# Optimization experiments

Hardware: AMD Instinct MI355X
Metric: run time of the kernel (lower is better)

The kernel has to match this reference:

```python
import jax, jax.numpy as jnp
import numpy as np

N_NODES = 100000
N_EDGES = 1600000
D = 128


def _graph_conv(x, src, dst, norm_src, norm_dst, W, b):
    # DGL GraphConv, norm='both': out = D_dst^{-1/2} A D_src^{-1/2} x W + b
    xs = x * norm_src[:, None]                 # [N, d] scale by src (out-)degree
    agg = jax.ops.segment_sum(xs[src], dst, num_segments=N_NODES)  # SpMM
    hd = agg * norm_dst[:, None]
    return hd @ W + b


def setup_inputs() -> dict:
    key = jax.random.key(0)
    ks = jax.random.split(key, 9)
    h = jax.random.normal(ks[0], (N_NODES, D), dtype=jnp.float32)
    src = jax.random.randint(ks[1], (N_EDGES,), 0, N_NODES, dtype=jnp.int64)
    dst = jax.random.randint(ks[2], (N_EDGES,), 0, N_NODES, dtype=jnp.int64)
    s = 1.0 / np.sqrt(D)
    W0 = jax.random.uniform(ks[3], (D, D), jnp.float32, -s, s)
    b0 = jnp.zeros((D,), jnp.float32)
    W1 = jax.random.uniform(ks[4], (D, D), jnp.float32, -s, s)
    b1 = jnp.zeros((D,), jnp.float32)
    W2 = jax.random.uniform(ks[5], (D, D), jnp.float32, -s, s)
    b2 = jnp.zeros((D,), jnp.float32)
    return {"h": h, "src": src, "dst": dst, "W0": W0, "b0": b0,
            "W1": W1, "b1": b1, "W2": W2, "b2": b2}


def reference(h, src, dst, W0, b0, W1, b1, W2, b2):
    ones = jnp.ones((N_EDGES,), jnp.float32)
    deg_out = jnp.maximum(jax.ops.segment_sum(ones, src, num_segments=N_NODES), 1.0)
    deg_in = jnp.maximum(jax.ops.segment_sum(ones, dst, num_segments=N_NODES), 1.0)
    norm_src = deg_out ** -0.5
    norm_dst = deg_in ** -0.5

    x = jax.nn.relu(_graph_conv(h, src, dst, norm_src, norm_dst, W0, b0))
    x = jax.nn.relu(_graph_conv(x, src, dst, norm_src, norm_dst, W1, b1))
    x = _graph_conv(x, src, dst, norm_src, norm_dst, W2, b2)
    # dgl.mean_nodes over a single graph -> [1, out_size]
    return jnp.mean(x, axis=0, keepdims=True)
```

## Files before the change

kernel.cpp:

```cpp
#include <hip/hip_runtime.h>
#include <hip/hip_fp16.h>

#define N_NODES 100000
#define N_EDGES 1600000
#define D 128
#define SCAN_NB ((N_NODES + 1023) / 1024)
#define CHK 128
#define CHUNK_E (N_EDGES / CHK)
#define HALF_N 50000
#define HALF_U (HALF_N / 4)
#define PP_STRIDE (N_NODES / 4)
#define NSH2 2
#define SH2 (N_NODES / NSH2)
#define SH2_U (SH2 / 4)

typedef _Float16 f16x4 __attribute__((ext_vector_type(4)));
typedef _Float16 f16x8 __attribute__((ext_vector_type(8)));
typedef float f32x4 __attribute__((ext_vector_type(4)));
typedef float f32x2 __attribute__((ext_vector_type(2)));

__global__ __launch_bounds__(256) void
k_hist(const int* __restrict__ src, const int* __restrict__ dst,
       unsigned int* __restrict__ pp) {
    __shared__ unsigned int h[HALF_U];
    int b = blockIdx.x;
    int arr = b >> 8, half = (b >> 7) & 1, c = b & (CHK - 1);
    const int* a = arr ? dst : src;
    int lo = half * HALF_N;
    for (int i = threadIdx.x; i < HALF_U; i += 256) h[i] = 0;
    __syncthreads();
    int e0 = c * CHUNK_E;
    for (int i = e0 + threadIdx.x; i < e0 + CHUNK_E; i += 256) {
        int v = a[i] - lo;
        if ((unsigned)v < HALF_N)
            atomicAdd(&h[v >> 2], 1u << ((v & 3) * 8));
    }
    __syncthreads();
    unsigned int* po = pp + ((size_t)(arr * CHK + c)) * PP_STRIDE + half * HALF_U;
    for (int i = threadIdx.x; i < HALF_U; i += 256) po[i] = h[i];
}

__global__ void k_merge(unsigned int* __restrict__ pp,
                        int* __restrict__ cnt_src, int* __restrict__ cnt_dst) {
    int g = blockIdx.x * blockDim.x + threadIdx.x;
    if (g >= 2 * PP_STRIDE) return;
    int arr = g / PP_STRIDE, u = g % PP_STRIDE;
    unsigned int* p = pp + ((size_t)arr * CHK) * PP_STRIDE + u;
    int s0 = 0, s1 = 0, s2 = 0, s3 = 0;
#pragma unroll 8
    for (int c = 0; c < CHK; c++) {
        unsigned int v = p[(size_t)c * PP_STRIDE];
        p[(size_t)c * PP_STRIDE] =
            (unsigned)s0 | ((unsigned)s1 << 8) | ((unsigned)s2 << 16) | ((unsigned)s3 << 24);
        s0 += v & 255; s1 += (v >> 8) & 255; s2 += (v >> 16) & 255; s3 += (v >> 24) & 255;
    }
    int* cnt = arr ? cnt_dst : cnt_src;
    cnt[4 * u + 0] = s0; cnt[4 * u + 1] = s1; cnt[4 * u + 2] = s2; cnt[4 * u + 3] = s3;
}

__global__ __launch_bounds__(1024) void
k_scan1(const int* __restrict__ cnt_dst, const int* __restrict__ cnt_src,
        int* __restrict__ rpD, int* __restrict__ rpS,
        int* __restrict__ bsD, int* __restrict__ bsS) {
    __shared__ int s[1024];
    int arr = blockIdx.x / SCAN_NB, bb = blockIdx.x % SCAN_NB;
    const int* cnt = arr ? cnt_src : cnt_dst;
    int* rp1 = (arr ? rpS : rpD) + 1;
    int* bs = arr ? bsS : bsD;
    int tid = threadIdx.x;
    int i = bb * 1024 + tid;
    int v = (i < N_NODES) ? cnt[i] : 0;
    s[tid] = v;
    __syncthreads();
    for (int d = 1; d < 1024; d <<= 1) {
        int t = (tid >= d) ? s[tid - d] : 0;
        __syncthreads();
        s[tid] += t;
        __syncthreads();
    }
    if (i < N_NODES) rp1[i] = s[tid];
    if (tid == 1023) bs[bb] = s[1023];
}

__global__ void k_scan2(int* __restrict__ bsD, int* __restrict__ bsS) {
    __shared__ int s[128];
    int* bs = blockIdx.x ? bsS : bsD;
    int tid = threadIdx.x;
    int v = (tid < SCAN_NB) ? bs[tid] : 0;
    s[tid] = v;
    __syncthreads();
    for (int d = 1; d < 128; d <<= 1) {
        int t = (tid >= d) ? s[tid - d] : 0;
        __syncthreads();
        s[tid] += t;
        __syncthreads();
    }
    if (tid < SCAN_NB) bs[tid] = s[tid] - v;
}

__global__ void k_scan3norm(int* __restrict__ rpD, int* __restrict__ rpS,
                            const int* __restrict__ bsD, const int* __restrict__ bsS,
                            const int* __restrict__ cnt_src, const int* __restrict__ cnt_dst,
                            float* __restrict__ ns, float* __restrict__ nd,
                            float* __restrict__ colsum) {
    int i = blockIdx.x * blockDim.x + threadIdx.x;
    if (i >= N_NODES) return;
    rpD[1 + i] += bsD[i >> 10];
    rpS[1 + i] += bsS[i >> 10];
    if (i == 0) { rpD[0] = 0; rpS[0] = 0; }
    if (i < 128) colsum[i] = 0.0f;
    ns[i] = rsqrtf((float)max(cnt_src[i], 1));
    nd[i] = rsqrtf((float)max(cnt_dst[i], 1));
}

__global__ __launch_bounds__(256) void
k_scatter_both(const int* __restrict__ src, const int* __restrict__ dst,
               const int* __restrict__ rpD, const int* __restrict__ rpS,
               const unsigned int* __restrict__ pp, const float* __restrict__ nd,
               int* __restrict__ csr_src, float* __restrict__ csrv) {
    __shared__ unsigned int cur[SH2_U];
    int which = blockIdx.x >> 8;
    int bb = blockIdx.x & 255;
    int sh = bb & 1, c = bb >> 1;
    int lo = sh * SH2;
    for (int i = threadIdx.x; i < SH2_U; i += 256) cur[i] = 0;
    __syncthreads();
    int e0 = c * CHUNK_E;
    if (which == 0) {
        const unsigned int* pre = pp + ((size_t)(CHK + c)) * PP_STRIDE;
        for (int i = e0 + threadIdx.x; i < e0 + CHUNK_E; i += 256) {
            int dfull = dst[i];
            int d = dfull - lo;
            if ((unsigned)d < SH2) {
                int sft = (d & 3) * 8;
                int rank = (atomicAdd(&cur[d >> 2], 1u << sft) >> sft) & 255;
                int p8 = (pre[dfull >> 2] >> ((dfull & 3) * 8)) & 255;
                csr_src[rpD[dfull] + p8 + rank] = src[i];
            }
        }
    } else {
        const unsigned int* pre = pp + (size_t)c * PP_STRIDE;
        for (int i = e0 + threadIdx.x; i < e0 + CHUNK_E; i += 256) {
            int sfull = src[i];
            int s = sfull - lo;
            if ((unsigned)s < SH2) {
                int sft = (s & 3) * 8;
                int rank = (atomicAdd(&cur[s >> 2], 1u << sft) >> sft) & 255;
                int p8 = (pre[sfull >> 2] >> ((sfull & 3) * 8)) & 255;
                csrv[rpS[sfull] + p8 + rank] = nd[dst[i]];
            }
        }
    }
}

__global__ void k_wsum(const int* __restrict__ rpS, const float* __restrict__ csrv,
                       const float* __restrict__ ns, float* __restrict__ wsum) {
    int gid = blockIdx.x * blockDim.x + threadIdx.x;
    int wv = gid >> 6, lane = gid & 63;
    int n = wv * 16 + (lane & 15);
    int off = lane >> 4;
    float s = 0.0f;
    int beg = 0, end = 0;
    if (n < N_NODES) { beg = rpS[n]; end = rpS[n + 1]; }
    for (int j = beg + off; j < end; j += 4) s += csrv[j];
    s += __shfl_xor(s, 16, 64);
    s += __shfl_xor(s, 32, 64);
    if (n < N_NODES && lane < 16) wsum[n] = s * ns[n];
}

__global__ void k_prep(const float* __restrict__ W0, const float* __restrict__ W1,
                       __half* __restrict__ Wt, const float* __restrict__ x,
                       const float* __restrict__ ns, unsigned int* __restrict__ out) {
    if (blockIdx.x < 128) {
        int i = blockIdx.x * 256 + threadIdx.x;
        int l = i >> 14, r = i & (D * D - 1);
        int n = r >> 7, k = r & 127;
        const float* W = l ? W1 : W0;
        Wt[i] = __float2half(W[k * D + n]);
        return;
    }
    int i = (blockIdx.x - 128) * 256 + threadIdx.x;
    if (i >= N_NODES * (D / 4)) return;
    int n = i >> 5;
    float4 v = ((const float4*)x)[i];
    float s = ns[n];
    int u = __builtin_amdgcn_cvt_pk_fp8_f32(v.x * s, v.y * s, 0, false);
    u = __builtin_amdgcn_cvt_pk_fp8_f32(v.z * s, v.w * s, u, true);
    out[i] = (unsigned int)u;
}

__global__ __launch_bounds__(256) void
k_spmm(const unsigned char* __restrict__ x8, const int* __restrict__ row_ptr,
       const int* __restrict__ csr_src, __half* __restrict__ agg) {
    int wave = (blockIdx.x * blockDim.x + threadIdx.x) >> 6;
    int lane = threadIdx.x & 63;
    int hf = lane >> 5, l32 = lane & 31;
    if (wave >= N_NODES) return;
    int beg = row_ptr[wave], end = row_ptr[wave + 1];
    float a0 = 0.f, a1 = 0.f, a2 = 0.f, a3 = 0.f;
    int j = beg;
    for (; j + 7 < end; j += 8) {
#pragma unroll
        for (int p = 0; p < 4; p++) {
            int s0 = csr_src[j + 2 * p];
            int s1 = csr_src[j + 2 * p + 1];
            int s = hf ? s1 : s0;
            unsigned int u = *(const unsigned int*)(x8 + (size_t)s * D + 4 * l32);
            f32x2 lo = __builtin_amdgcn_cvt_pk_f32_fp8(u, false);
            f32x2 hi = __builtin_amdgcn_cvt_pk_f32_fp8(u, true);
            a0 += lo[0]; a1 += lo[1]; a2 += hi[0]; a3 += hi[1];
        }
    }
    for (; j + 1 < end; j += 2) {
        int s0 = csr_src[j], s1 = csr_src[j + 1];
        int s = hf ? s1 : s0;
        unsigned int u = *(const unsigned int*)(x8 + (size_t)s * D + 4 * l32);
        f32x2 lo = __builtin_amdgcn_cvt_pk_f32_fp8(u, false);
        f32x2 hi = __builtin_amdgcn_cvt_pk_f32_fp8(u, true);
        a0 += lo[0]; a1 += lo[1]; a2 += hi[0]; a3 += hi[1];
    }
    if (j < end && hf == 0) {
        int s = csr_src[j];
        unsigned int u = *(const unsigned int*)(x8 + (size_t)s * D + 4 * l32);
        f32x2 lo = __builtin_amdgcn_cvt_pk_f32_fp8(u, false);
        f32x2 hi = __builtin_amdgcn_cvt_pk_f32_fp8(u, true);
        a0 += lo[0]; a1 += lo[1]; a2 += hi[0]; a3 += hi[1];
    }
    a0 += __shfl_xor(a0, 32, 64);
    a1 += __shfl_xor(a1, 32, 64);
    a2 += __shfl_xor(a2, 32, 64);
    a3 += __shfl_xor(a3, 32, 64);
    if (hf == 0) {
        f16x4 o;
        o[0] = (_Float16)a0; o[1] = (_Float16)a1; o[2] = (_Float16)a2; o[3] = (_Float16)a3;
        ((f16x4*)(agg + (size_t)wave * D))[l32] = o;
    }
}

__global__ __launch_bounds__(256) void
k_gemm_mfma(const __half* __restrict__ A, const __half* __restrict__ Wt,
            const float* __restrict__ b, const float* __restrict__ nd,
            const float* __restrict__ ns, unsigned char* __restrict__ out) {
    int w = threadIdx.x >> 6, lane = threadIdx.x & 63;
    int m = lane & 15, q = lane >> 4;
    int row0 = blockIdx.x * 128 + w * 32;

    f16x8 zf;
#pragma unroll
    for (int j = 0; j < 8; j++) zf[j] = (_Float16)0;
    f16x8 af[2][4];
#pragma unroll
    for (int g = 0; g < 2; g++) {
        int arow = row0 + g * 16 + m;
        const f16x8* pa = (const f16x8*)(A + (size_t)arow * D);
        bool aok = arow < N_NODES;
#pragma unroll
        for (int ks = 0; ks < 4; ks++) af[g][ks] = aok ? pa[ks * 4 + q] : zf;
    }

    const f16x8* pb = (const f16x8*)Wt;
    f32x4 acc[2][8];
#pragma unroll
    for (int g = 0; g < 2; g++)
#pragma unroll
        for (int nt = 0; nt < 8; nt++) acc[g][nt] = (f32x4){0.f, 0.f, 0.f, 0.f};

#pragma unroll
    for (int ks = 0; ks < 4; ks++) {
#pragma unroll
        for (int nt = 0; nt < 8; nt++) {
            f16x8 bf = pb[((nt * 16 + m) << 4) + (ks << 2) + q];
            acc[0][nt] = __builtin_amdgcn_mfma_f32_16x16x32_f16(af[0][ks], bf, acc[0][nt], 0, 0, 0);
            acc[1][nt] = __builtin_amdgcn_mfma_f32_16x16x32_f16(af[1][ks], bf, acc[1][nt], 0, 0, 0);
        }
    }

#pragma unroll
    for (int g = 0; g < 2; g++) {
        int er = row0 + g * 16 + q * 4;
        float sd[4], ss[4];
#pragma unroll
        for (int r = 0; r < 4; r++) {
            int n = er + r;
            bool ok = n < N_NODES;
            sd[r] = ok ? nd[n] : 0.0f;
            ss[r] = ok ? ns[n] : 0.0f;
        }
#pragma unroll
        for (int nt = 0; nt < 8; nt++) {
            int col = nt * 16 + m;
            float bc = b[col];
#pragma unroll
            for (int r = 0; r < 4; r++) {
                int n = er + r;
                if (n < N_NODES) {
                    float v = fmaxf(sd[r] * acc[g][nt][r] + bc, 0.0f) * ss[r];
                    int pk = __builtin_amdgcn_cvt_pk_fp8_f32(v, v, 0, false);
                    out[(size_t)n * D + col] = (unsigned char)(pk & 0xff);
                }
            }
        }
    }
}

__global__ __launch_bounds__(256) void
k_gemm_red(const __half* __restrict__ A, const __half* __restrict__ Wt,
           const float* __restrict__ b, const float* __restrict__ nd,
           const float* __restrict__ wsum, float* __restrict__ colsum) {
    __shared__ float red[128];
    int tid = threadIdx.x;
    if (tid < 128) red[tid] = 0.0f;
    __syncthreads();

    int w = tid >> 6, lane = tid & 63;
    int m = lane & 15, q = lane >> 4;
    int row0 = blockIdx.x * 128 + w * 32;

    f16x8 zf;
#pragma unroll
    for (int j = 0; j < 8; j++) zf[j] = (_Float16)0;
    f16x8 af[2][4];
#pragma unroll
    for (int g = 0; g < 2; g++) {
        int arow = row0 + g * 16 + m;
        const f16x8* pa = (const f16x8*)(A + (size_t)arow * D);
        bool aok = arow < N_NODES;
#pragma unroll
        for (int ks = 0; ks < 4; ks++) af[g][ks] = aok ? pa[ks * 4 + q] : zf;
    }

    const f16x8* pb = (const f16x8*)Wt;
    f32x4 acc[2][8];
#pragma unroll
    for (int g = 0; g < 2; g++)
#pragma unroll
        for (int nt = 0; nt < 8; nt++) acc[g][nt] = (f32x4){0.f, 0.f, 0.f, 0.f};

#pragma unroll
    for (int ks = 0; ks < 4; ks++) {
#pragma unroll
        for (int nt = 0; nt < 8; nt++) {
            f16x8 bf = pb[((nt * 16 + m) << 4) + (ks << 2) + q];
            acc[0][nt] = __builtin_amdgcn_mfma_f32_16x16x32_f16(af[0][ks], bf, acc[0][nt], 0, 0, 0);
            acc[1][nt] = __builtin_amdgcn_mfma_f32_16x16x32_f16(af[1][ks], bf, acc[1][nt], 0, 0, 0);
        }
    }

    float sd[2][4], sw[2][4];
#pragma unroll
    for (int g = 0; g < 2; g++) {
        int er = row0 + g * 16 + q * 4;
#pragma unroll
        for (int r = 0; r < 4; r++) {
            int n = er + r;
            bool ok = n < N_NODES;
            sd[g][r] = ok ? nd[n] : 0.0f;
            sw[g][r] = ok ? wsum[n] : 0.0f;
        }
    }
#pragma unroll
    for (int nt = 0; nt < 8; nt++) {
        int col = nt * 16 + m;
        float bc = b[col];
        float pc = 0.0f;
#pragma unroll
        for (int g = 0; g < 2; g++)
#pragma unroll
            for (int r = 0; r < 4; r++)
                pc += sw[g][r] * fmaxf(sd[g][r] * acc[g][nt][r] + bc, 0.0f);
        atomicAdd(&red[col], pc);
    }
    __syncthreads();
    if (tid < 128) unsafeAtomicAdd(&colsum[tid], red[tid]);
}

__global__ void k_final(const float* __restrict__ colsum, const float* __restrict__ W,
                        const float* __restrict__ b, float* __restrict__ out) {
    __shared__ float m[128];
    int j = threadIdx.x;
    m[j] = colsum[j] * (1.0f / N_NODES);
    __syncthreads();
    float acc = b[j];
    for (int k = 0; k < 128; k++)
        acc = fmaf(m[k], W[(size_t)k * D + j], acc);
    out[j] = acc;
}

extern "C" void kernel_launch(void* const* d_in, const int* in_sizes, int n_in,
                              void* d_out, int out_size, void* d_ws, size_t ws_size,
                              hipStream_t stream) {
    const float* h   = (const float*)d_in[0];
    const int*   src = (const int*)d_in[1];
    const int*   dst = (const int*)d_in[2];
    const float* W0  = (const float*)d_in[3];
    const float* b0  = (const float*)d_in[4];
    const float* W1  = (const float*)d_in[5];
    const float* b1  = (const float*)d_in[6];
    const float* W2  = (const float*)d_in[7];
    const float* b2  = (const float*)d_in[8];
    float* out = (float*)d_out;

    float*         ns      = (float*)d_ws;
    float*         nd      = ns + N_NODES;
    float*         wsum    = nd + N_NODES;
    float*         colsum  = wsum + N_NODES;
    int*           rpD     = (int*)(colsum + 128);
    int*           rpS     = rpD + N_NODES + 1;
    int*           cnt_src = rpS + N_NODES + 1;
    int*           cnt_dst = cnt_src + N_NODES;
    int*           bsD     = cnt_dst + N_NODES;
    int*           bsS     = bsD + 128;
    __half*        Wt16    = (__half*)(bsS + 128);
    int*           csr_src = (int*)(Wt16 + 2 * D * D);
    float*         csrv    = (float*)(csr_src + N_EDGES);
    unsigned int*  pp      = (unsigned int*)(csrv + N_EDGES);
    unsigned char* x8      = (unsigned char*)pp;
    __half*        agg16   = (__half*)(pp + 2 * (size_t)CHK * PP_STRIDE);

    k_hist<<<2 * 2 * CHK, 256, 0, stream>>>(src, dst, pp);
    k_merge<<<(2 * PP_STRIDE + 255) / 256, 256, 0, stream>>>(pp, cnt_src, cnt_dst);
    k_scan1<<<2 * SCAN_NB, 1024, 0, stream>>>(cnt_dst, cnt_src, rpD, rpS, bsD, bsS);
    k_scan2<<<2, 128, 0, stream>>>(bsD, bsS);
    k_scan3norm<<<(N_NODES + 255) / 256, 256, 0, stream>>>(rpD, rpS, bsD, bsS,
                                                           cnt_src, cnt_dst, ns, nd, colsum);
    k_scatter_both<<<2 * NSH2 * CHK, 256, 0, stream>>>(src, dst, rpD, rpS, pp, nd,
                                                       csr_src, csrv);
    k_wsum<<<(N_NODES * 4 + 255) / 256, 256, 0, stream>>>(rpS, csrv, ns, wsum);

    k_prep<<<128 + (N_NODES * (D / 4) + 255) / 256, 256, 0, stream>>>(
        W0, W1, Wt16, h, ns, (unsigned int*)x8);

    k_spmm<<<(N_NODES + 3) / 4, 256, 0, stream>>>(x8, rpD, csr_src, agg16);
    k_gemm_mfma<<<(N_NODES + 127) / 128, 256, 0, stream>>>(agg16, Wt16, b0, nd, ns, x8);
    k_spmm<<<(N_NODES + 3) / 4, 256, 0, stream>>>(x8, rpD, csr_src, agg16);
    k_gemm_red<<<(N_NODES + 127) / 128, 256, 0, stream>>>(agg16, Wt16 + (size_t)D * D,
                                                          b1, nd, wsum, colsum);
    k_final<<<1, 128, 0, stream>>>(colsum, W2, b2, out);
}
```

Measured before the change: 429.8 us.

## Replace chunked histogram CSR build with global atomic degree count and scatter

Drops the per-chunk packed-byte LDS histograms, the merge pass, and the source-side CSR. Degrees now come from global atomics, the scan runs on the destination side only, and edges are scattered with atomic cursors. The weighted out-degree sum (wsum) is built directly with float atomics during the scatter, so k_wsum and the csrv array go away, and the ns factor moves into k_gemm_red. This cuts kernel launches and memory traffic. In exchange, edge order within each CSR row becomes nondeterministic, float atomic order varies between runs, and there may be contention on global atomics.

```diff
diff --git a/kernel.cpp b/kernel.cpp
--- a/kernel.cpp
+++ b/kernel.cpp
@@ -5,14 +5,6 @@
 #define N_EDGES 1600000
 #define D 128
 #define SCAN_NB ((N_NODES + 1023) / 1024)
-#define CHK 128
-#define CHUNK_E (N_EDGES / CHK)
-#define HALF_N 50000
-#define HALF_U (HALF_N / 4)
-#define PP_STRIDE (N_NODES / 4)
-#define NSH2 2
-#define SH2 (N_NODES / NSH2)
-#define SH2_U (SH2 / 4)
 
 typedef _Float16 f16x4 __attribute__((ext_vector_type(4)));
 typedef _Float16 f16x8 __attribute__((ext_vector_type(8)));
@@ -20,157 +12,8 @@
 typedef float f32x2 __attribute__((ext_vector_type(2)));
 
 __global__ __launch_bounds__(256) void
-k_hist(const int* __restrict__ src, const int* __restrict__ dst,
-       unsigned int* __restrict__ pp) {
-    __shared__ unsigned int h[HALF_U];
-    int b = blockIdx.x;
-    int arr = b >> 8, half = (b >> 7) & 1, c = b & (CHK - 1);
-    const int* a = arr ? dst : src;
-    int lo = half * HALF_N;
-    for (int i = threadIdx.x; i < HALF_U; i += 256) h[i] = 0;
-    __syncthreads();
-    int e0 = c * CHUNK_E;
-    for (int i = e0 + threadIdx.x; i < e0 + CHUNK_E; i += 256) {
-        int v = a[i] - lo;
-        if ((unsigned)v < HALF_N)
-            atomicAdd(&h[v >> 2], 1u << ((v & 3) * 8));
-    }
-    __syncthreads();
-    unsigned int* po = pp + ((size_t)(arr * CHK + c)) * PP_STRIDE + half * HALF_U;
-    for (int i = threadIdx.x; i < HALF_U; i += 256) po[i] = h[i];
-}
-
-__global__ void k_merge(unsigned int* __restrict__ pp,
-                        int* __restrict__ cnt_src, int* __restrict__ cnt_dst) {
-    int g = blockIdx.x * blockDim.x + threadIdx.x;
-    if (g >= 2 * PP_STRIDE) return;
-    int arr = g / PP_STRIDE, u = g % PP_STRIDE;
-    unsigned int* p = pp + ((size_t)arr * CHK) * PP_STRIDE + u;
-    int s0 = 0, s1 = 0, s2 = 0, s3 = 0;
-#pragma unroll 8
-    for (int c = 0; c < CHK; c++) {
-        unsigned int v = p[(size_t)c * PP_STRIDE];
-        p[(size_t)c * PP_STRIDE] =
-            (unsigned)s0 | ((unsigned)s1 << 8) | ((unsigned)s2 << 16) | ((unsigned)s3 << 24);
-        s0 += v & 255; s1 += (v >> 8) & 255; s2 += (v >> 16) & 255; s3 += (v >> 24) & 255;
-    }
-    int* cnt = arr ? cnt_dst : cnt_src;
-    cnt[4 * u + 0] = s0; cnt[4 * u + 1] = s1; cnt[4 * u + 2] = s2; cnt[4 * u + 3] = s3;
-}
-
-__global__ __launch_bounds__(1024) void
-k_scan1(const int* __restrict__ cnt_dst, const int* __restrict__ cnt_src,
-        int* __restrict__ rpD, int* __restrict__ rpS,
-        int* __restrict__ bsD, int* __restrict__ bsS) {
-    __shared__ int s[1024];
-    int arr = blockIdx.x / SCAN_NB, bb = blockIdx.x % SCAN_NB;
-    const int* cnt = arr ? cnt_src : cnt_dst;
-    int* rp1 = (arr ? rpS : rpD) + 1;
-    int* bs = arr ? bsS : bsD;
-    int tid = threadIdx.x;
-    int i = bb * 1024 + tid;
-    int v = (i < N_NODES) ? cnt[i] : 0;
-    s[tid] = v;
-    __syncthreads();
-    for (int d = 1; d < 1024; d <<= 1) {
-        int t = (tid >= d) ? s[tid - d] : 0;
-        __syncthreads();
-        s[tid] += t;
-        __syncthreads();
-    }
-    if (i < N_NODES) rp1[i] = s[tid];
-    if (tid == 1023) bs[bb] = s[1023];
-}
-
-__global__ void k_scan2(int* __restrict__ bsD, int* __restrict__ bsS) {
-    __shared__ int s[128];
-    int* bs = blockIdx.x ? bsS : bsD;
-    int tid = threadIdx.x;
-    int v = (tid < SCAN_NB) ? bs[tid] : 0;
-    s[tid] = v;
-    __syncthreads();
-    for (int d = 1; d < 128; d <<= 1) {
-        int t = (tid >= d) ? s[tid - d] : 0;
-        __syncthreads();
-        s[tid] += t;
-        __syncthreads();
-    }
-    if (tid < SCAN_NB) bs[tid] = s[tid] - v;
-}
-
-__global__ void k_scan3norm(int* __restrict__ rpD, int* __restrict__ rpS,
-                            const int* __restrict__ bsD, const int* __restrict__ bsS,
-                            const int* __restrict__ cnt_src, const int* __restrict__ cnt_dst,
-                            float* __restrict__ ns, float* __restrict__ nd,
-                            float* __restrict__ colsum) {
-    int i = blockIdx.x * blockDim.x + threadIdx.x;
-    if (i >= N_NODES) return;
-    rpD[1 + i] += bsD[i >> 10];
-    rpS[1 + i] += bsS[i >> 10];
-    if (i == 0) { rpD[0] = 0; rpS[0] = 0; }
-    if (i < 128) colsum[i] = 0.0f;
-    ns[i] = rsqrtf((float)max(cnt_src[i], 1));
-    nd[i] = rsqrtf((float)max(cnt_dst[i], 1));
-}
-
-__global__ __launch_bounds__(256) void
-k_scatter_both(const int* __restrict__ src, const int* __restrict__ dst,
-               const int* __restrict__ rpD, const int* __restrict__ rpS,
-               const unsigned int* __restrict__ pp, const float* __restrict__ nd,
-               int* __restrict__ csr_src, float* __restrict__ csrv) {
-    __shared__ unsigned int cur[SH2_U];
-    int which = blockIdx.x >> 8;
-    int bb = blockIdx.x & 255;
-    int sh = bb & 1, c = bb >> 1;
-    int lo = sh * SH2;
-    for (int i = threadIdx.x; i < SH2_U; i += 256) cur[i] = 0;
-    __syncthreads();
-    int e0 = c * CHUNK_E;
-    if (which == 0) {
-        const unsigned int* pre = pp + ((size_t)(CHK + c)) * PP_STRIDE;
-        for (int i = e0 + threadIdx.x; i < e0 + CHUNK_E; i += 256) {
-            int dfull = dst[i];
-            int d = dfull - lo;
-            if ((unsigned)d < SH2) {
-                int sft = (d & 3) * 8;
-                int rank = (atomicAdd(&cur[d >> 2], 1u << sft) >> sft) & 255;
-                int p8 = (pre[dfull >> 2] >> ((dfull & 3) * 8)) & 255;
-                csr_src[rpD[dfull] + p8 + rank] = src[i];
-            }
-        }
-    } else {
-        const unsigned int* pre = pp + (size_t)c * PP_STRIDE;
-        for (int i = e0 + threadIdx.x; i < e0 + CHUNK_E; i += 256) {
-            int sfull = src[i];
-            int s = sfull - lo;
-            if ((unsigned)s < SH2) {
-                int sft = (s & 3) * 8;
-                int rank = (atomicAdd(&cur[s >> 2], 1u << sft) >> sft) & 255;
-                int p8 = (pre[sfull >> 2] >> ((sfull & 3) * 8)) & 255;
-                csrv[rpS[sfull] + p8 + rank] = nd[dst[i]];
-            }
-        }
-    }
-}
-
-__global__ void k_wsum(const int* __restrict__ rpS, const float* __restrict__ csrv,
-                       const float* __restrict__ ns, float* __restrict__ wsum) {
-    int gid = blockIdx.x * blockDim.x + threadIdx.x;
-    int wv = gid >> 6, lane = gid & 63;
-    int n = wv * 16 + (lane & 15);
-    int off = lane >> 4;
-    float s = 0.0f;
-    int beg = 0, end = 0;
-    if (n < N_NODES) { beg = rpS[n]; end = rpS[n + 1]; }
-    for (int j = beg + off; j < end; j += 4) s += csrv[j];
-    s += __shfl_xor(s, 16, 64);
-    s += __shfl_xor(s, 32, 64);
-    if (n < N_NODES && lane < 16) wsum[n] = s * ns[n];
-}
-
-__global__ void k_prep(const float* __restrict__ W0, const float* __restrict__ W1,
-                       __half* __restrict__ Wt, const float* __restrict__ x,
-                       const float* __restrict__ ns, unsigned int* __restrict__ out) {
+k_zwt(const float* __restrict__ W0, const float* __restrict__ W1,
+      __half* __restrict__ Wt, uint4* __restrict__ zbase) {
     if (blockIdx.x < 128) {
         int i = blockIdx.x * 256 + threadIdx.x;
         int l = i >> 14, r = i & (D * D - 1);
@@ -180,6 +23,96 @@
         return;
     }
     int i = (blockIdx.x - 128) * 256 + threadIdx.x;
+    if (i < 3 * N_NODES / 4) zbase[i] = (uint4){0u, 0u, 0u, 0u};
+}
+
+__global__ __launch_bounds__(256) void
+k_deg(const int* __restrict__ src, const int* __restrict__ dst,
+      int* __restrict__ cnt_src, int* __restrict__ cnt_dst) {
+    int i = blockIdx.x * 256 + threadIdx.x;
+    if (i >= N_EDGES / 4) return;
+    int4 s = ((const int4*)src)[i];
+    int4 d = ((const int4*)dst)[i];
+    atomicAdd(&cnt_src[s.x], 1); atomicAdd(&cnt_src[s.y], 1);
+    atomicAdd(&cnt_src[s.z], 1); atomicAdd(&cnt_src[s.w], 1);
+    atomicAdd(&cnt_dst[d.x], 1); atomicAdd(&cnt_dst[d.y], 1);
+    atomicAdd(&cnt_dst[d.z], 1); atomicAdd(&cnt_dst[d.w], 1);
+}
+
+__global__ __launch_bounds__(1024) void
+k_scan1(const int* __restrict__ cnt_dst, int* __restrict__ rpD,
+        int* __restrict__ bsD) {
+    __shared__ int s[1024];
+    int tid = threadIdx.x;
+    int i = blockIdx.x * 1024 + tid;
+    int v = (i < N_NODES) ? cnt_dst[i] : 0;
+    s[tid] = v;
+    __syncthreads();
+    for (int d = 1; d < 1024; d <<= 1) {
+        int t = (tid >= d) ? s[tid - d] : 0;
+        __syncthreads();
+        s[tid] += t;
+        __syncthreads();
+    }
+    if (i < N_NODES) rpD[1 + i] = s[tid];
+    if (tid == 1023) bsD[blockIdx.x] = s[1023];
+}
+
+__global__ void k_scan2(int* __restrict__ bs) {
+    __shared__ int s[128];
+    int tid = threadIdx.x;
+    int v = (tid < SCAN_NB) ? bs[tid] : 0;
+    s[tid] = v;
+    __syncthreads();
+    for (int d = 1; d < 128; d <<= 1) {
+        int t = (tid >= d) ? s[tid - d] : 0;
+        __syncthreads();
+        s[tid] += t;
+        __syncthreads();
+    }
+    if (tid < SCAN_NB) bs[tid] = s[tid] - v;
+}
+
+__global__ void k_scan3norm(int* __restrict__ rpD, const int* __restrict__ bsD,
+                            const int* __restrict__ cnt_src,
+                            const int* __restrict__ cnt_dst,
+                            float* __restrict__ ns, float* __restrict__ nd,
+                            int* __restrict__ cur, float* __restrict__ colsum) {
+    int i = blockIdx.x * blockDim.x + threadIdx.x;
+    if (i >= N_NODES) return;
+    int c = cnt_dst[i];
+    int v = rpD[1 + i] + bsD[i >> 10];
+    rpD[1 + i] = v;
+    cur[i] = v - c;
+    if (i == 0) rpD[0] = 0;
+    if (i < 128) colsum[i] = 0.0f;
+    ns[i] = rsqrtf((float)max(cnt_src[i], 1));
+    nd[i] = rsqrtf((float)max(cnt_dst[i], 1));
+}
+
+__global__ __launch_bounds__(256) void
+k_scatter(const int* __restrict__ src, const int* __restrict__ dst,
+          int* __restrict__ cur, const float* __restrict__ nd,
+          int* __restrict__ csr_src, float* __restrict__ wsum) {
+    int i = blockIdx.x * 256 + threadIdx.x;
+    if (i >= N_EDGES / 4) return;
+    int4 s = ((const int4*)src)[i];
+    int4 d = ((const int4*)dst)[i];
+    int p0 = atomicAdd(&cur[d.x], 1);
+    int p1 = atomicAdd(&cur[d.y], 1);
+    int p2 = atomicAdd(&cur[d.z], 1);
+    int p3 = atomicAdd(&cur[d.w], 1);
+    csr_src[p0] = s.x; csr_src[p1] = s.y;
+    csr_src[p2] = s.z; csr_src[p3] = s.w;
+    unsafeAtomicAdd(&wsum[s.x], nd[d.x]);
+    unsafeAtomicAdd(&wsum[s.y], nd[d.y]);
+    unsafeAtomicAdd(&wsum[s.z], nd[d.z]);
+    unsafeAtomicAdd(&wsum[s.w], nd[d.w]);
+}
+
+__global__ void k_prep(const float* __restrict__ x, const float* __restrict__ ns,
+                       unsigned int* __restrict__ out) {
+    int i = blockIdx.x * 256 + threadIdx.x;
     if (i >= N_NODES * (D / 4)) return;
     int n = i >> 5;
     float4 v = ((const float4*)x)[i];
@@ -306,7 +239,8 @@
 __global__ __launch_bounds__(256) void
 k_gemm_red(const __half* __restrict__ A, const __half* __restrict__ Wt,
            const float* __restrict__ b, const float* __restrict__ nd,
-           const float* __restrict__ wsum, float* __restrict__ colsum) {
+           const float* __restrict__ ns, const float* __restrict__ wsum,
+           float* __restrict__ colsum) {
     __shared__ float red[128];
     int tid = threadIdx.x;
     if (tid < 128) red[tid] = 0.0f;
@@ -355,7 +289,7 @@
             int n = er + r;
             bool ok = n < N_NODES;
             sd[g][r] = ok ? nd[n] : 0.0f;
-            sw[g][r] = ok ? wsum[n] : 0.0f;
+            sw[g][r] = ok ? wsum[n] * ns[n] : 0.0f;
         }
     }
 #pragma unroll
@@ -400,40 +334,36 @@
     const float* b2  = (const float*)d_in[8];
     float* out = (float*)d_out;
 
-    float*         ns      = (float*)d_ws;
+    int*           cnt_src = (int*)d_ws;
+    int*           cnt_dst = cnt_src + N_NODES;
+    float*         wsum    = (float*)(cnt_dst + N_NODES);
+    float*         ns      = wsum + N_NODES;
     float*         nd      = ns + N_NODES;
-    float*         wsum    = nd + N_NODES;
-    float*         colsum  = wsum + N_NODES;
-    int*           rpD     = (int*)(colsum + 128);
-    int*           rpS     = rpD + N_NODES + 1;
-    int*           cnt_src = rpS + N_NODES + 1;
-    int*           cnt_dst = cnt_src + N_NODES;
-    int*           bsD     = cnt_dst + N_NODES;
-    int*           bsS     = bsD + 128;
-    __half*        Wt16    = (__half*)(bsS + 128);
+    int*           cur     = (int*)(nd + N_NODES);
+    float*         colsum  = (float*)(cur + N_NODES);
+    int*           bsD     = (int*)(colsum + 128);
+    int*           rpD     = bsD + 128;
+    __half*        Wt16    = (__half*)(rpD + N_NODES + 4);
     int*           csr_src = (int*)(Wt16 + 2 * D * D);
-    float*         csrv    = (float*)(csr_src + N_EDGES);
-    unsigned int*  pp      = (unsigned int*)(csrv + N_EDGES);
-    unsigned char* x8      = (unsigned char*)pp;
-    __half*        agg16   = (__half*)(pp + 2 * (size_t)CHK * PP_STRIDE);
-
-    k_hist<<<2 * 2 * CHK, 256, 0, stream>>>(src, dst, pp);
-    k_merge<<<(2 * PP_STRIDE + 255) / 256, 256, 0, stream>>>(pp, cnt_src, cnt_dst);
-    k_scan1<<<2 * SCAN_NB, 1024, 0, stream>>>(cnt_dst, cnt_src, rpD, rpS, bsD, bsS);
-    k_scan2<<<2, 128, 0, stream>>>(bsD, bsS);
-    k_scan3norm<<<(N_NODES + 255) / 256, 256, 0, stream>>>(rpD, rpS, bsD, bsS,
-                                                           cnt_src, cnt_dst, ns, nd, colsum);
-    k_scatter_both<<<2 * NSH2 * CHK, 256, 0, stream>>>(src, dst, rpD, rpS, pp, nd,
-                                                       csr_src, csrv);
-    k_wsum<<<(N_NODES * 4 + 255) / 256, 256, 0, stream>>>(rpS, csrv, ns, wsum);
-
-    k_prep<<<128 + (N_NODES * (D / 4) + 255) / 256, 256, 0, stream>>>(
-        W0, W1, Wt16, h, ns, (unsigned int*)x8);
+    unsigned char* x8      = (unsigned char*)(csr_src + N_EDGES);
+    __half*        agg16   = (__half*)(x8 + (size_t)N_NODES * D);
+
+    k_zwt<<<128 + (3 * N_NODES / 4 + 255) / 256, 256, 0, stream>>>(
+        W0, W1, Wt16, (uint4*)d_ws);
+    k_deg<<<(N_EDGES / 4 + 255) / 256, 256, 0, stream>>>(src, dst, cnt_src, cnt_dst);
+    k_scan1<<<SCAN_NB, 1024, 0, stream>>>(cnt_dst, rpD, bsD);
+    k_scan2<<<1, 128, 0, stream>>>(bsD);
+    k_scan3norm<<<(N_NODES + 255) / 256, 256, 0, stream>>>(rpD, bsD, cnt_src,
+                                                           cnt_dst, ns, nd, cur, colsum);
+    k_scatter<<<(N_EDGES / 4 + 255) / 256, 256, 0, stream>>>(src, dst, cur, nd,
+                                                             csr_src, wsum);
+
+    k_prep<<<(N_NODES * (D / 4) + 255) / 256, 256, 0, stream>>>(h, ns, (unsigned int*)x8);
 
     k_spmm<<<(N_NODES + 3) / 4, 256, 0, stream>>>(x8, rpD, csr_src, agg16);
     k_gemm_mfma<<<(N_NODES + 127) / 128, 256, 0, stream>>>(agg16, Wt16, b0, nd, ns, x8);
     k_spmm<<<(N_NODES + 3) / 4, 256, 0, stream>>>(x8, rpD, csr_src, agg16);
     k_gemm_red<<<(N_NODES + 127) / 128, 256, 0, stream>>>(agg16, Wt16 + (size_t)D * D,
-                                                          b1, nd, wsum, colsum);
+                                                          b1, nd, ns, wsum, colsum);
     k_final<<<1, 128, 0, stream>>>(colsum, W2, b2, out);
 }
```

New measurement: 596.5 us. +38.8%, slower.
